# Kernel optimization log

Hardware: AMD Instinct MI355X
Metric: run time of the kernel (lower is better)

The kernel has to match this reference:

```python
import jax, jax.numpy as jnp
import numpy as np

N_NODES = 100000
N_EDGES = 3200000
D = 32


def setup_inputs() -> dict:
    key = jax.random.key(0)
    k = jax.random.split(key, 5)
    x = jax.random.normal(k[0], (N_NODES, D), dtype=jnp.float32)
    edge_index = jax.random.randint(k[1], (2, N_EDGES), 0, N_NODES, dtype=jnp.int64)
    W1 = jax.random.normal(k[2], (D, D), dtype=jnp.float32) * (1.0 / np.sqrt(D))
    b1 = jnp.zeros((D,), dtype=jnp.float32)
    W2 = jax.random.normal(k[3], (D, D), dtype=jnp.float32) * (1.0 / np.sqrt(D))
    b2 = jnp.zeros((D,), dtype=jnp.float32)
    return {"x": x, "edge_index": edge_index, "W1": W1, "b1": b1, "W2": W2, "b2": b2}


def reference(x, edge_index, W1, b1, W2, b2):
    n = x.shape[0]
    # add self-loops (PyG GCNConv default)
    loop = jnp.arange(n, dtype=edge_index.dtype)
    src = jnp.concatenate([edge_index[0], loop])
    dst = jnp.concatenate([edge_index[1], loop])
    # symmetric normalization: deg computed on dst with self-loops; deg >= 1 so no inf handling needed
    deg = jax.ops.segment_sum(jnp.ones_like(src, dtype=x.dtype), dst, num_segments=n)
    dinv = jax.lax.rsqrt(deg)
    norm = (dinv[src] * dinv[dst])[:, None]  # [E+N, 1]

    def gcn_layer(h, W, b):
        h = h @ W.T                                        # dense transform [N, D]
        msg = h[src] * norm                                # gather + scale   [E+N, D]
        agg = jax.ops.segment_sum(msg, dst, num_segments=n)  # scatter-add  [N, D]
        return jax.nn.relu(agg + b)

    h = gcn_layer(x, W1, b1)
    h = gcn_layer(h, W2, b2)
    return h
```

## Files before the change

### kernel.cpp

```cpp
#include <hip/hip_runtime.h>

#define THREADS 256
#define BIGT 1024
#define NBLK 256
#define BSHIFT 8
#define BSZ (1 << BSHIFT)
#define MAXB 512

__global__ void detect_kernel(const unsigned int* ei_words, int* flag_int64, long long n_words) {
    __shared__ int nonzero;
    if (threadIdx.x == 0) nonzero = 0;
    __syncthreads();
    long long w = 2LL * threadIdx.x + 1;
    if (w < n_words) {
        if (ei_words[w] != 0u) atomicOr(&nonzero, 1);
    }
    __syncthreads();
    if (threadIdx.x == 0) *flag_int64 = (nonzero == 0) ? 1 : 0;
}

__global__ __launch_bounds__(BIGT) void bin_count_kernel(
        const void* __restrict__ ei, const int* __restrict__ flag_int64,
        int* __restrict__ blockhist, int E, int NB) {
    __shared__ int h[MAXB];
    int tid = threadIdx.x;
    for (int i = tid; i < NB; i += blockDim.x) h[i] = 0;
    __syncthreads();
    int chunk = (E + gridDim.x - 1) / gridDim.x;
    int s = blockIdx.x * chunk;
    int e = min(E, s + chunk);
    if (*flag_int64) {
        const long long* p = (const long long*)ei;
        for (int i = s + tid; i < e; i += blockDim.x)
            atomicAdd(&h[(int)p[E + i] >> BSHIFT], 1);
    } else {
        const int* p = (const int*)ei;
        for (int i = s + tid; i < e; i += blockDim.x)
            atomicAdd(&h[p[E + i] >> BSHIFT], 1);
    }
    __syncthreads();
    for (int i = tid; i < NB; i += blockDim.x)
        blockhist[i * NBLK + blockIdx.x] = h[i];
}

__global__ __launch_bounds__(BIGT) void bin_write_kernel(
        const void* __restrict__ ei, const int* __restrict__ flag_int64,
        const int* __restrict__ offsets, unsigned int* __restrict__ ebuf,
        int E, int NB) {
    __shared__ int cur[MAXB];
    int tid = threadIdx.x;
    for (int i = tid; i < NB; i += blockDim.x)
        cur[i] = offsets[i * NBLK + blockIdx.x];
    __syncthreads();
    int chunk = (E + gridDim.x - 1) / gridDim.x;
    int s = blockIdx.x * chunk;
    int e = min(E, s + chunk);
    if (*flag_int64) {
        const long long* p = (const long long*)ei;
        for (int i = s + tid; i < e; i += blockDim.x) {
            int d = (int)p[E + i];
            int sr = (int)p[i];
            int pos = atomicAdd(&cur[d >> BSHIFT], 1);
            ebuf[pos] = ((unsigned int)(d & (BSZ - 1)) << 20) | (unsigned int)sr;
        }
    } else {
        const int* p = (const int*)ei;
        for (int i = s + tid; i < e; i += blockDim.x) {
            int d = p[E + i];
            int sr = p[i];
            int pos = atomicAdd(&cur[d >> BSHIFT], 1);
            ebuf[pos] = ((unsigned int)(d & (BSZ - 1)) << 20) | (unsigned int)sr;
        }
    }
}

__global__ void scan_blocks_kernel(const int* __restrict__ cnt, int* __restrict__ ofs,
                                   int* __restrict__ partials, int T) {
    __shared__ int sd[THREADS];
    int tid = threadIdx.x;
    int base = blockIdx.x * 1024 + tid * 4;
    int c0 = (base + 0 < T) ? cnt[base + 0] : 0;
    int c1 = (base + 1 < T) ? cnt[base + 1] : 0;
    int c2 = (base + 2 < T) ? cnt[base + 2] : 0;
    int c3 = (base + 3 < T) ? cnt[base + 3] : 0;
    int tsum = c0 + c1 + c2 + c3;
    sd[tid] = tsum;
    __syncthreads();
    for (int off = 1; off < THREADS; off <<= 1) {
        int t = (tid >= off) ? sd[tid - off] : 0;
        __syncthreads();
        sd[tid] += t;
        __syncthreads();
    }
    int excl = sd[tid] - tsum;
    if (base + 0 < T) ofs[base + 0] = excl;
    if (base + 1 < T) ofs[base + 1] = excl + c0;
    if (base + 2 < T) ofs[base + 2] = excl + c0 + c1;
    if (base + 3 < T) ofs[base + 3] = excl + c0 + c1 + c2;
    if (tid == THREADS - 1) partials[blockIdx.x] = sd[tid];
}

__global__ void scan_partials_kernel(int* __restrict__ partials, int* __restrict__ total_out, int B) {
    __shared__ int sd[128];
    int tid = threadIdx.x;
    int v = (tid < B) ? partials[tid] : 0;
    sd[tid] = v;
    __syncthreads();
    for (int off = 1; off < 128; off <<= 1) {
        int t = (tid >= off) ? sd[tid - off] : 0;
        __syncthreads();
        sd[tid] += t;
        __syncthreads();
    }
    if (tid < B) partials[tid] = sd[tid] - v;
    if (tid == 127) total_out[0] = sd[127];
}

__global__ void scan_add_kernel(int* __restrict__ ofs, const int* __restrict__ partials, int T) {
    int tid = threadIdx.x;
    int base = blockIdx.x * 1024 + tid * 4;
    int add = partials[blockIdx.x];
    if (base + 0 < T) ofs[base + 0] += add;
    if (base + 1 < T) ofs[base + 1] += add;
    if (base + 2 < T) ofs[base + 2] += add;
    if (base + 3 < T) ofs[base + 3] += add;
}

__global__ __launch_bounds__(BIGT) void place_kernel(
        const unsigned int* __restrict__ ebuf, const int* __restrict__ offsets,
        int* __restrict__ rowptr, float* __restrict__ dinv, int* __restrict__ col,
        int N, int NB) {
    __shared__ int cnt[BSZ];
    __shared__ int scanbuf[BSZ];
    __shared__ int baseL[BSZ];
    __shared__ int fillL[BSZ];
    int b = blockIdx.x;
    int lo = b << BSHIFT;
    int tid = threadIdx.x;
    if (tid < BSZ) cnt[tid] = 0;
    __syncthreads();
    int start = offsets[b * NBLK];
    int end   = offsets[(b + 1) * NBLK];
    for (int p = start + tid; p < end; p += BIGT)
        atomicAdd(&cnt[(ebuf[p] >> 20) & (BSZ - 1)], 1);
    __syncthreads();
    int c = (tid < BSZ) ? cnt[tid] : 0;
    if (tid < BSZ) scanbuf[tid] = c;
    __syncthreads();
    for (int off = 1; off < BSZ; off <<= 1) {
        int t = (tid < BSZ && tid >= off) ? scanbuf[tid - off] : 0;
        __syncthreads();
        if (tid < BSZ) scanbuf[tid] += t;
        __syncthreads();
    }
    if (tid < BSZ) {
        int excl = scanbuf[tid] - c;
        int node = lo + tid;
        if (node < N) {
            rowptr[node] = start + excl;
            dinv[node] = 1.0f / sqrtf((float)(c + 1));
            if (node == N - 1) rowptr[N] = start + excl + c;
        }
        baseL[tid] = start + excl;
        fillL[tid] = 0;
    }
    __syncthreads();
    for (int p = start + tid; p < end; p += BIGT) {
        unsigned int v = ebuf[p];
        int dl = (v >> 20) & (BSZ - 1);
        int pos = baseL[dl] + atomicAdd(&fillL[dl], 1);
        col[pos] = (int)(v & 0xFFFFFu);
    }
}

__global__ void dense_kernel(const float* __restrict__ h, const float* __restrict__ W,
                             const float* __restrict__ dinv, float* __restrict__ out, int N) {
    __shared__ float Wt[1024];
    __shared__ float hs[THREADS];
    int tid = threadIdx.x;
    for (int idx = tid; idx < 1024; idx += THREADS) {
        int r = idx >> 5, c = idx & 31;
        Wt[c * 32 + r] = W[idx];
    }
    int gid = blockIdx.x * THREADS + tid;
    int total = N * 32;
    if (gid < total) hs[tid] = h[gid];
    __syncthreads();
    if (gid >= total) return;
    int ln = tid >> 5;
    int j = tid & 31;
    const float* hr = hs + ln * 32;
    float s = 0.f;
#pragma unroll
    for (int k = 0; k < 32; ++k) s = fmaf(hr[k], Wt[k * 32 + j], s);
    out[gid] = s * dinv[gid >> 5];
}

__global__ void agg_kernel(const float* __restrict__ ht, const int* __restrict__ rowptr,
                           const int* __restrict__ col, const float* __restrict__ dinv,
                           const float* __restrict__ bias, float* __restrict__ out, int N) {
    int gid = blockIdx.x * THREADS + threadIdx.x;
    int n = gid >> 5;
    if (n >= N) return;
    int j = gid & 31;
    float s = ht[gid];
    int p = rowptr[n], end = rowptr[n + 1];
    for (; p + 8 <= end; p += 8) {
        int c0 = col[p], c1 = col[p + 1], c2 = col[p + 2], c3 = col[p + 3];
        int c4 = col[p + 4], c5 = col[p + 5], c6 = col[p + 6], c7 = col[p + 7];
        float v0 = ht[c0 * 32 + j];
        float v1 = ht[c1 * 32 + j];
        float v2 = ht[c2 * 32 + j];
        float v3 = ht[c3 * 32 + j];
        float v4 = ht[c4 * 32 + j];
        float v5 = ht[c5 * 32 + j];
        float v6 = ht[c6 * 32 + j];
        float v7 = ht[c7 * 32 + j];
        s += ((v0 + v1) + (v2 + v3)) + ((v4 + v5) + (v6 + v7));
    }
    for (; p + 4 <= end; p += 4) {
        int c0 = col[p], c1 = col[p + 1], c2 = col[p + 2], c3 = col[p + 3];
        float v0 = ht[c0 * 32 + j];
        float v1 = ht[c1 * 32 + j];
        float v2 = ht[c2 * 32 + j];
        float v3 = ht[c3 * 32 + j];
        s += (v0 + v1) + (v2 + v3);
    }
    for (; p < end; ++p) s += ht[col[p] * 32 + j];
    out[gid] = fmaxf(fmaf(dinv[n], s, bias[j]), 0.f);
}

extern "C" void kernel_launch(void* const* d_in, const int* in_sizes, int n_in,
                              void* d_out, int out_size, void* d_ws, size_t ws_size,
                              hipStream_t stream) {
    const float* x  = (const float*)d_in[0];
    const void*  ei = d_in[1];
    const float* W1 = (const float*)d_in[2];
    const float* b1 = (const float*)d_in[3];
    const float* W2 = (const float*)d_in[4];
    const float* b2 = (const float*)d_in[5];
    float* out = (float*)d_out;

    int N = in_sizes[0] / 32;
    long long twoE = (long long)in_sizes[1];
    int E = (int)(twoE / 2);
    int NB = (N + BSZ - 1) >> BSHIFT;
    int T  = NB * NBLK;

    char* ws = (char*)d_ws;
    size_t o = 0;
    auto alloc = [&](size_t bytes) { size_t r = o; o += (bytes + 255) & ~(size_t)255; return r; };
    int*   flag      = (int*)(ws + alloc(4));
    int*   blockhist = (int*)(ws + alloc((size_t)T * 4));
    int*   offsets   = (int*)(ws + alloc((size_t)(T + 1) * 4));
    int*   rowptr    = (int*)(ws + alloc((size_t)(N + 1) * 4));
    int*   partials  = (int*)(ws + alloc(512));
    float* dinv      = (float*)(ws + alloc((size_t)N * 4));
    unsigned int* ebuf = (unsigned int*)(ws + alloc((size_t)E * 4));
    int*   col       = (int*)(ws + alloc((size_t)E * 4));
    float* ht        = (float*)(ws + alloc((size_t)N * 32 * 4));
    float* h1        = (float*)(ws + alloc((size_t)N * 32 * 4));

    detect_kernel<<<1, 256, 0, stream>>>((const unsigned int*)ei, flag, twoE);

    bin_count_kernel<<<NBLK, BIGT, 0, stream>>>(ei, flag, blockhist, E, NB);

    int SB = (T + 1023) / 1024;
    scan_blocks_kernel<<<SB, THREADS, 0, stream>>>(blockhist, offsets, partials, T);
    scan_partials_kernel<<<1, 128, 0, stream>>>(partials, offsets + T, SB);
    scan_add_kernel<<<SB, THREADS, 0, stream>>>(offsets, partials, T);

    bin_write_kernel<<<NBLK, BIGT, 0, stream>>>(ei, flag, offsets, ebuf, E, NB);
    place_kernel<<<NB, BIGT, 0, stream>>>(ebuf, offsets, rowptr, dinv, col, N, NB);

    int GB = (N * 32 + THREADS - 1) / THREADS;
    dense_kernel<<<GB, THREADS, 0, stream>>>(x, W1, dinv, ht, N);
    agg_kernel<<<GB, THREADS, 0, stream>>>(ht, rowptr, col, dinv, b1, h1, N);
    dense_kernel<<<GB, THREADS, 0, stream>>>(h1, W2, dinv, ht, N);
    agg_kernel<<<GB, THREADS, 0, stream>>>(ht, rowptr, col, dinv, b2, out, N);
}
```

Before: 313.3 us.

## Fuse scan stages, first dense into placement, and second dense into aggregation

Result: faster. 272.8 us (-12.9%).

```diff
diff --git a/kernel.cpp b/kernel.cpp
--- a/kernel.cpp
+++ b/kernel.cpp
@@ -100,44 +100,44 @@
     if (tid == THREADS - 1) partials[blockIdx.x] = sd[tid];
 }
 
-__global__ void scan_partials_kernel(int* __restrict__ partials, int* __restrict__ total_out, int B) {
+__global__ void scan_add2_kernel(int* __restrict__ ofs, const int* __restrict__ partials,
+                                 int T, int SB) {
     __shared__ int sd[128];
     int tid = threadIdx.x;
-    int v = (tid < B) ? partials[tid] : 0;
-    sd[tid] = v;
+    if (tid < 128) sd[tid] = (tid < SB) ? partials[tid] : 0;
     __syncthreads();
     for (int off = 1; off < 128; off <<= 1) {
-        int t = (tid >= off) ? sd[tid - off] : 0;
-        __syncthreads();
-        sd[tid] += t;
-        __syncthreads();
-    }
-    if (tid < B) partials[tid] = sd[tid] - v;
-    if (tid == 127) total_out[0] = sd[127];
-}
-
-__global__ void scan_add_kernel(int* __restrict__ ofs, const int* __restrict__ partials, int T) {
-    int tid = threadIdx.x;
+        int t = (tid < 128 && tid >= off) ? sd[tid - off] : 0;
+        __syncthreads();
+        if (tid < 128) sd[tid] += t;
+        __syncthreads();
+    }
+    int add = (blockIdx.x > 0) ? sd[blockIdx.x - 1] : 0;
     int base = blockIdx.x * 1024 + tid * 4;
-    int add = partials[blockIdx.x];
     if (base + 0 < T) ofs[base + 0] += add;
     if (base + 1 < T) ofs[base + 1] += add;
     if (base + 2 < T) ofs[base + 2] += add;
     if (base + 3 < T) ofs[base + 3] += add;
-}
-
-__global__ __launch_bounds__(BIGT) void place_kernel(
+    if (blockIdx.x == gridDim.x - 1 && tid == 0) ofs[T] = sd[SB - 1];
+}
+
+__global__ __launch_bounds__(BIGT) void place_dense_kernel(
         const unsigned int* __restrict__ ebuf, const int* __restrict__ offsets,
+        const float* __restrict__ x, const float* __restrict__ W1,
         int* __restrict__ rowptr, float* __restrict__ dinv, int* __restrict__ col,
-        int N, int NB) {
+        float* __restrict__ ht1, int N, int NB) {
     __shared__ int cnt[BSZ];
     __shared__ int scanbuf[BSZ];
     __shared__ int baseL[BSZ];
     __shared__ int fillL[BSZ];
+    __shared__ float dinvL[BSZ];
+    __shared__ float Wt[1024];
+    __shared__ float xs[BIGT];
     int b = blockIdx.x;
     int lo = b << BSHIFT;
     int tid = threadIdx.x;
     if (tid < BSZ) cnt[tid] = 0;
+    Wt[(tid & 31) * 32 + (tid >> 5)] = W1[tid];
     __syncthreads();
     int start = offsets[b * NBLK];
     int end   = offsets[(b + 1) * NBLK];
@@ -156,9 +156,11 @@
     if (tid < BSZ) {
         int excl = scanbuf[tid] - c;
         int node = lo + tid;
+        float dv = 1.0f / sqrtf((float)(c + 1));
+        dinvL[tid] = dv;
         if (node < N) {
             rowptr[node] = start + excl;
-            dinv[node] = 1.0f / sqrtf((float)(c + 1));
+            dinv[node] = dv;
             if (node == N - 1) rowptr[N] = start + excl + c;
         }
         baseL[tid] = start + excl;
@@ -171,62 +173,111 @@
         int pos = baseL[dl] + atomicAdd(&fillL[dl], 1);
         col[pos] = (int)(v & 0xFFFFFu);
     }
-}
-
-__global__ void dense_kernel(const float* __restrict__ h, const float* __restrict__ W,
-                             const float* __restrict__ dinv, float* __restrict__ out, int N) {
+    __syncthreads();
+    for (int base0 = 0; base0 < BSZ * 32; base0 += BIGT) {
+        int idx = base0 + tid;
+        int ln = idx >> 5;
+        int node = lo + ln;
+        xs[tid] = (node < N) ? x[(size_t)lo * 32 + idx] : 0.f;
+        __syncthreads();
+        if (node < N) {
+            int j = idx & 31;
+            const float* xr = xs + ((tid >> 5) << 5);
+            float s = 0.f;
+#pragma unroll
+            for (int k = 0; k < 32; ++k) s = fmaf(xr[k], Wt[k * 32 + j], s);
+            ht1[(size_t)node * 32 + j] = s * dinvL[ln];
+        }
+        __syncthreads();
+    }
+}
+
+__global__ __launch_bounds__(THREADS) void agg_dense_kernel(
+        const float* __restrict__ ht1, const int* __restrict__ rowptr,
+        const int* __restrict__ col, const float* __restrict__ dinv,
+        const float* __restrict__ b1, const float* __restrict__ W2,
+        float* __restrict__ ht2, int N) {
     __shared__ float Wt[1024];
-    __shared__ float hs[THREADS];
-    int tid = threadIdx.x;
-    for (int idx = tid; idx < 1024; idx += THREADS) {
-        int r = idx >> 5, c = idx & 31;
-        Wt[c * 32 + r] = W[idx];
-    }
+    __shared__ float hr[THREADS];
+    int tid = threadIdx.x;
+    for (int idx = tid; idx < 1024; idx += THREADS)
+        Wt[(idx & 31) * 32 + (idx >> 5)] = W2[idx];
     int gid = blockIdx.x * THREADS + tid;
-    int total = N * 32;
-    if (gid < total) hs[tid] = h[gid];
-    __syncthreads();
-    if (gid >= total) return;
-    int ln = tid >> 5;
-    int j = tid & 31;
-    const float* hr = hs + ln * 32;
-    float s = 0.f;
+    int n = gid >> 5;
+    int j = gid & 31;
+    bool act = (n < N);
+    float h1v = 0.f, dv = 0.f;
+    if (act) {
+        dv = dinv[n];
+        float s = ht1[gid];
+        int p = rowptr[n], end = rowptr[n + 1];
+        for (; p + 8 <= end; p += 8) {
+            int c0 = col[p], c1 = col[p + 1], c2 = col[p + 2], c3 = col[p + 3];
+            int c4 = col[p + 4], c5 = col[p + 5], c6 = col[p + 6], c7 = col[p + 7];
+            float v0 = ht1[c0 * 32 + j];
+            float v1 = ht1[c1 * 32 + j];
+            float v2 = ht1[c2 * 32 + j];
+            float v3 = ht1[c3 * 32 + j];
+            float v4 = ht1[c4 * 32 + j];
+            float v5 = ht1[c5 * 32 + j];
+            float v6 = ht1[c6 * 32 + j];
+            float v7 = ht1[c7 * 32 + j];
+            s += ((v0 + v1) + (v2 + v3)) + ((v4 + v5) + (v6 + v7));
+        }
+        for (; p + 4 <= end; p += 4) {
+            int c0 = col[p], c1 = col[p + 1], c2 = col[p + 2], c3 = col[p + 3];
+            float v0 = ht1[c0 * 32 + j];
+            float v1 = ht1[c1 * 32 + j];
+            float v2 = ht1[c2 * 32 + j];
+            float v3 = ht1[c3 * 32 + j];
+            s += (v0 + v1) + (v2 + v3);
+        }
+        for (; p < end; ++p) s += ht1[col[p] * 32 + j];
+        h1v = fmaxf(fmaf(dv, s, b1[j]), 0.f);
+    }
+    hr[tid] = h1v;
+    __syncthreads();
+    if (act) {
+        const float* hrow = hr + ((tid >> 5) << 5);
+        float t = 0.f;
 #pragma unroll
-    for (int k = 0; k < 32; ++k) s = fmaf(hr[k], Wt[k * 32 + j], s);
-    out[gid] = s * dinv[gid >> 5];
-}
-
-__global__ void agg_kernel(const float* __restrict__ ht, const int* __restrict__ rowptr,
-                           const int* __restrict__ col, const float* __restrict__ dinv,
-                           const float* __restrict__ bias, float* __restrict__ out, int N) {
+        for (int k = 0; k < 32; ++k) t = fmaf(hrow[k], Wt[k * 32 + j], t);
+        ht2[gid] = t * dv;
+    }
+}
+
+__global__ __launch_bounds__(THREADS) void agg_final_kernel(
+        const float* __restrict__ ht2, const int* __restrict__ rowptr,
+        const int* __restrict__ col, const float* __restrict__ dinv,
+        const float* __restrict__ bias, float* __restrict__ out, int N) {
     int gid = blockIdx.x * THREADS + threadIdx.x;
     int n = gid >> 5;
     if (n >= N) return;
     int j = gid & 31;
-    float s = ht[gid];
+    float s = ht2[gid];
     int p = rowptr[n], end = rowptr[n + 1];
     for (; p + 8 <= end; p += 8) {
         int c0 = col[p], c1 = col[p + 1], c2 = col[p + 2], c3 = col[p + 3];
         int c4 = col[p + 4], c5 = col[p + 5], c6 = col[p + 6], c7 = col[p + 7];
-        float v0 = ht[c0 * 32 + j];
-        float v1 = ht[c1 * 32 + j];
-        float v2 = ht[c2 * 32 + j];
-        float v3 = ht[c3 * 32 + j];
-        float v4 = ht[c4 * 32 + j];
-        float v5 = ht[c5 * 32 + j];
-        float v6 = ht[c6 * 32 + j];
-        float v7 = ht[c7 * 32 + j];
+        float v0 = ht2[c0 * 32 + j];
+        float v1 = ht2[c1 * 32 + j];
+        float v2 = ht2[c2 * 32 + j];
+        float v3 = ht2[c3 * 32 + j];
+        float v4 = ht2[c4 * 32 + j];
+        float v5 = ht2[c5 * 32 + j];
+        float v6 = ht2[c6 * 32 + j];
+        float v7 = ht2[c7 * 32 + j];
         s += ((v0 + v1) + (v2 + v3)) + ((v4 + v5) + (v6 + v7));
     }
     for (; p + 4 <= end; p += 4) {
         int c0 = col[p], c1 = col[p + 1], c2 = col[p + 2], c3 = col[p + 3];
-        float v0 = ht[c0 * 32 + j];
-        float v1 = ht[c1 * 32 + j];
-        float v2 = ht[c2 * 32 + j];
-        float v3 = ht[c3 * 32 + j];
+        float v0 = ht2[c0 * 32 + j];
+        float v1 = ht2[c1 * 32 + j];
+        float v2 = ht2[c2 * 32 + j];
+        float v3 = ht2[c3 * 32 + j];
         s += (v0 + v1) + (v2 + v3);
     }
-    for (; p < end; ++p) s += ht[col[p] * 32 + j];
+    for (; p < end; ++p) s += ht2[col[p] * 32 + j];
     out[gid] = fmaxf(fmaf(dinv[n], s, bias[j]), 0.f);
 }
 
@@ -258,8 +309,8 @@
     float* dinv      = (float*)(ws + alloc((size_t)N * 4));
     unsigned int* ebuf = (unsigned int*)(ws + alloc((size_t)E * 4));
     int*   col       = (int*)(ws + alloc((size_t)E * 4));
-    float* ht        = (float*)(ws + alloc((size_t)N * 32 * 4));
-    float* h1        = (float*)(ws + alloc((size_t)N * 32 * 4));
+    float* ht1       = (float*)(ws + alloc((size_t)N * 32 * 4));
+    float* ht2       = (float*)(ws + alloc((size_t)N * 32 * 4));
 
     detect_kernel<<<1, 256, 0, stream>>>((const unsigned int*)ei, flag, twoE);
 
@@ -267,15 +318,12 @@
 
     int SB = (T + 1023) / 1024;
     scan_blocks_kernel<<<SB, THREADS, 0, stream>>>(blockhist, offsets, partials, T);
-    scan_partials_kernel<<<1, 128, 0, stream>>>(partials, offsets + T, SB);
-    scan_add_kernel<<<SB, THREADS, 0, stream>>>(offsets, partials, T);
+    scan_add2_kernel<<<SB, THREADS, 0, stream>>>(offsets, partials, T, SB);
 
     bin_write_kernel<<<NBLK, BIGT, 0, stream>>>(ei, flag, offsets, ebuf, E, NB);
-    place_kernel<<<NB, BIGT, 0, stream>>>(ebuf, offsets, rowptr, dinv, col, N, NB);
+    place_dense_kernel<<<NB, BIGT, 0, stream>>>(ebuf, offsets, x, W1, rowptr, dinv, col, ht1, N, NB);
 
     int GB = (N * 32 + THREADS - 1) / THREADS;
-    dense_kernel<<<GB, THREADS, 0, stream>>>(x, W1, dinv, ht, N);
-    agg_kernel<<<GB, THREADS, 0, stream>>>(ht, rowptr, col, dinv, b1, h1, N);
-    dense_kernel<<<GB, THREADS, 0, stream>>>(h1, W2, dinv, ht, N);
-    agg_kernel<<<GB, THREADS, 0, stream>>>(ht, rowptr, col, dinv, b2, out, N);
-}
+    agg_dense_kernel<<<GB, THREADS, 0, stream>>>(ht1, rowptr, col, dinv, b1, W2, ht2, N);
+    agg_final_kernel<<<GB, THREADS, 0, stream>>>(ht2, rowptr, col, dinv, b2, out, N);
+}
```
